# Kernel tuning notes

Hardware: AMD Instinct MI355X
Metric: run time of the kernel (lower is better)

Reference implementation:

```python
import jax, jax.numpy as jnp
import numpy as np

B, T, I, H = 1024, 2048, 12, 512


def setup_inputs() -> dict:
    key = jax.random.key(0)
    k1, k2, k3, k4 = jax.random.split(key, 4)
    s = 1.0 / np.sqrt(H)
    return {
        "history": jax.random.normal(k1, (B, T, I), dtype=jnp.float32),
        "w_ih": jax.random.normal(k2, (3 * H, I), dtype=jnp.float32) * s,
        "w_hh": jax.random.normal(k3, (3 * H, H), dtype=jnp.float32) * s,
        "w_out": jax.random.normal(k4, (2, H), dtype=jnp.float32) * s,
        "b_out": jnp.zeros((2,), dtype=jnp.float32),
    }


def reference(history, w_ih, w_hh, w_out, b_out):
    # GRUCell recurrence over T steps with per-step linear head (torch GRUCell math, bias=False)
    xs = jnp.transpose(history, (1, 0, 2))  # [T, B, I]
    h0 = jnp.zeros((history.shape[0], H), dtype=history.dtype)

    def step(h, x_t):
        gi = x_t @ w_ih.T            # [B, 3H]
        gh = h @ w_hh.T              # [B, 3H]
        i_r, i_z, i_n = jnp.split(gi, 3, axis=-1)
        h_r, h_z, h_n = jnp.split(gh, 3, axis=-1)
        r = jax.nn.sigmoid(i_r + h_r)
        z = jax.nn.sigmoid(i_z + h_z)
        n = jnp.tanh(i_n + r * h_n)
        h_new = (1.0 - z) * n + z * h
        logit = h_new @ w_out.T + b_out  # [B, 2]
        return h_new, logit

    h_final, logits = jax.lax.scan(step, h0, xs)
    return jnp.transpose(logits, (1, 0, 2)), h_final  # ([B, T, 2], [B, H])
```

## Files before the change

### kernel.cpp

```cpp
#include <hip/hip_runtime.h>
#include <stdint.h>


#define NB 256
#define NT 256
#define TB 1024
#define TT 2048
#define II 12
#define HH 512
#define NCL 32
#define GBLK 8
#define ROWS 32

#define HTILE_B (ROWS * HH * 2)
#define HBUF_B  ((size_t)NCL * HTILE_B)
#define BAR_OFF ((size_t)2 * HBUF_B)
#define WS_USED (BAR_OFF + (size_t)NCL * 256)

#define LDSB (ROWS * 1024)

#define GAS __attribute__((address_space(1)))
#define LAS __attribute__((address_space(3)))

typedef _Float16 half8 __attribute__((ext_vector_type(8)));
typedef float    f32x4 __attribute__((ext_vector_type(4)));

static __device__ __forceinline__ float fast_sigmoid(float x) {
  float e = exp2f(-1.44269504f * x);
  return __builtin_amdgcn_rcpf(1.0f + e);
}
static __device__ __forceinline__ float fast_tanh(float x) {
  float e = exp2f(2.88539008f * x);
  return 1.0f - 2.0f * __builtin_amdgcn_rcpf(1.0f + e);
}

static __device__ __forceinline__ void wait_flags32(unsigned* f, unsigned tgt,
                                                    int* dead) {
  const int l = threadIdx.x & 63;
  long spin = 0;
  for (;;) {
    unsigned v = __hip_atomic_load(f + (l & 31), __ATOMIC_RELAXED,
                                   __HIP_MEMORY_SCOPE_AGENT);
    if (__all(v >= tgt)) break;
    if (++spin > (1L << 24)) { *dead = 1; break; }
  }
}

__global__ void __launch_bounds__(NT, 1)
gru_persistent(const float* __restrict__ hist,
               const float* __restrict__ w_ih,
               const float* __restrict__ w_hh,
               const float* __restrict__ w_out,
               const float* __restrict__ b_out,
               float* __restrict__ out,
               uint8_t* __restrict__ ws)
{
  extern __shared__ char smem[];
  char* ldsA = smem;
  const int bid = blockIdx.x;
  const int c   = bid & 31;
  const int g   = bid >> 5;
  const int tid = threadIdx.x;
  const int w   = tid >> 6;
  const int l   = tid & 63;
  const int l15 = l & 15;
  const int l4  = l >> 4;
  const int crb = c * ROWS;
  unsigned* loF = (unsigned*)(ws + BAR_OFF) + (size_t)c * 64;
  unsigned* hiF = loF + 32;
  const int myflag = g * 4 + w;

  const int col0 = g * 64 + w * 16;

  half8 wr[16], wz[16], wn[16];
#pragma unroll
  for (int ks = 0; ks < 16; ++ks) {
    const size_t Rr = (size_t)(0 * HH + col0 + l15) * HH + ks * 32 + l4 * 8;
    const size_t Rz = (size_t)(1 * HH + col0 + l15) * HH + ks * 32 + l4 * 8;
    const size_t Rn = (size_t)(2 * HH + col0 + l15) * HH + ks * 32 + l4 * 8;
#pragma unroll
    for (int i = 0; i < 8; ++i) {
      wr[ks][i] = (_Float16)w_hh[Rr + i];
      wz[ks][i] = (_Float16)w_hh[Rz + i];
      wn[ks][i] = (_Float16)w_hh[Rn + i];
    }
  }

  half8 wih[3];
#pragma unroll
  for (int gt = 0; gt < 3; ++gt) {
    const int R = gt * HH + col0 + l15;
#pragma unroll
    for (int i = 0; i < 8; ++i) {
      const int k = l4 * 8 + i;
      wih[gt][i] = (_Float16)((k < II) ? w_ih[R * II + k] : 0.0f);
    }
  }

  const int jj = (l >> 4) & 1;
  float wor[32];
#pragma unroll
  for (int i = 0; i < 32; ++i) wor[i] = w_out[jj * HH + l15 * 32 + i];
  const float bo = b_out[jj];

  float hprev[2][4];
#pragma unroll
  for (int mt = 0; mt < 2; ++mt)
#pragma unroll
    for (int q = 0; q < 4; ++q) hprev[mt][q] = 0.0f;

  const int pcol = col0 + l15;
  int deadlock = 0;

  f32x4 xn0[2], xn1[2];
#pragma unroll
  for (int mt = 0; mt < 2; ++mt) {
    xn0[mt] = (f32x4){0.f, 0.f, 0.f, 0.f};
    xn1[mt] = (f32x4){0.f, 0.f, 0.f, 0.f};
    const float* xp = hist + (size_t)(crb + mt * 16 + l15) * (TT * II);
    if (l4 == 0)      { xn0[mt] = *(const f32x4*)xp; xn1[mt] = *(const f32x4*)(xp + 4); }
    else if (l4 == 1) { xn0[mt] = *(const f32x4*)(xp + 8); }
  }

  unsigned preLo = 0, preHi = 0;

  for (int t = 0; t < TT; ++t) {
    const uint8_t* hsrc = ws + ((t & 1) ? HBUF_B : 0) + (size_t)c * HTILE_B;
    uint8_t*       hdst = ws + ((t & 1) ? 0 : HBUF_B) + (size_t)c * HTILE_B;

    if (!__all(preLo >= (unsigned)t)) wait_flags32(loF, (unsigned)t, &deadlock);
    __builtin_amdgcn_sched_barrier(0);

#pragma unroll
    for (int it = 0; it < 4; ++it)
      __builtin_amdgcn_global_load_lds(
          (const GAS uint32_t*)(hsrc + it * 4096 + tid * 16),
          (LAS uint32_t*)(ldsA + it * 4096 + tid * 16), 16, 0, 17);
    __builtin_amdgcn_sched_barrier(0);

    half8 ax[2];
#pragma unroll
    for (int mt = 0; mt < 2; ++mt)
#pragma unroll
      for (int i = 0; i < 4; ++i) {
        ax[mt][i]     = (_Float16)xn0[mt][i];
        ax[mt][4 + i] = (_Float16)xn1[mt][i];
      }
    {
      const int tx = (t + 1 < TT) ? (t + 1) : 0;
#pragma unroll
      for (int mt = 0; mt < 2; ++mt) {
        const float* xp = hist + (size_t)(crb + mt * 16 + l15) * (TT * II) + (size_t)tx * II;
        if (l4 == 0)      { xn0[mt] = *(const f32x4*)xp; xn1[mt] = *(const f32x4*)(xp + 4); }
        else if (l4 == 1) { xn0[mt] = *(const f32x4*)(xp + 8); }
      }
    }
    preHi = __hip_atomic_load(hiF + (l & 31), __ATOMIC_RELAXED,
                              __HIP_MEMORY_SCOPE_AGENT);
    __builtin_amdgcn_sched_barrier(0);

    asm volatile("s_waitcnt vmcnt(7)" ::: "memory");
    __builtin_amdgcn_s_barrier();
    __builtin_amdgcn_sched_barrier(0);

    f32x4 acc0 = (f32x4){0.f, 0.f, 0.f, 0.f};
    f32x4 acc1 = acc0, acc2 = acc0;
    f32x4 accin = __builtin_amdgcn_mfma_f32_16x16x32_f16(ax[0], wih[2],
                    (f32x4){0.f, 0.f, 0.f, 0.f}, 0, 0, 0);
    acc0 = __builtin_amdgcn_mfma_f32_16x16x32_f16(ax[0], wih[0], acc0, 0, 0, 0);
    acc1 = __builtin_amdgcn_mfma_f32_16x16x32_f16(ax[0], wih[1], acc1, 0, 0, 0);
#pragma unroll
    for (int ks = 0; ks < 16; ++ks) {
      const int ko = (ks * 64 + l4 * 16) ^ ((l15 & 7) << 4);
      half8 a = *(const half8*)(ldsA + l15 * 1024 + ko);
      acc0 = __builtin_amdgcn_mfma_f32_16x16x32_f16(a, wr[ks], acc0, 0, 0, 0);
      acc1 = __builtin_amdgcn_mfma_f32_16x16x32_f16(a, wz[ks], acc1, 0, 0, 0);
      acc2 = __builtin_amdgcn_mfma_f32_16x16x32_f16(a, wn[ks], acc2, 0, 0, 0);
    }

    if (!__all(preHi >= (unsigned)t)) wait_flags32(hiF, (unsigned)t, &deadlock);
    __builtin_amdgcn_sched_barrier(0);
#pragma unroll
    for (int it = 0; it < 4; ++it)
      __builtin_amdgcn_global_load_lds(
          (const GAS uint32_t*)(hsrc + 16384 + it * 4096 + tid * 16),
          (LAS uint32_t*)(ldsA + 16384 + it * 4096 + tid * 16), 16, 0, 17);
    __builtin_amdgcn_sched_barrier(0);

#pragma unroll
    for (int q = 0; q < 4; ++q) {
      const int m = l4 * 4 + q;
      const float r  = fast_sigmoid(acc0[q]);
      const float z  = fast_sigmoid(acc1[q]);
      const float n  = fast_tanh(accin[q] + r * acc2[q]);
      const float hn = (1.0f - z) * n + z * hprev[0][q];
      hprev[0][q] = hn;
      const unsigned short hu = __builtin_bit_cast(unsigned short, (_Float16)hn);
      __hip_atomic_store(
          (unsigned short*)(hdst + m * 1024 + ((pcol * 2) ^ ((m & 7) << 4))),
          hu, __ATOMIC_RELAXED, __HIP_MEMORY_SCOPE_AGENT);
    }
    __builtin_amdgcn_sched_barrier(0);

    asm volatile("s_waitcnt vmcnt(0)" ::: "memory");
    if (l == 0)
      __hip_atomic_store(loF + myflag, (unsigned)(t + 1), __ATOMIC_RELAXED,
                         __HIP_MEMORY_SCOPE_AGENT);
    __builtin_amdgcn_s_barrier();
    __builtin_amdgcn_sched_barrier(0);

    acc0 = (f32x4){0.f, 0.f, 0.f, 0.f};
    acc1 = acc0; acc2 = acc0;
    accin = __builtin_amdgcn_mfma_f32_16x16x32_f16(ax[1], wih[2],
              (f32x4){0.f, 0.f, 0.f, 0.f}, 0, 0, 0);
    acc0 = __builtin_amdgcn_mfma_f32_16x16x32_f16(ax[1], wih[0], acc0, 0, 0, 0);
    acc1 = __builtin_amdgcn_mfma_f32_16x16x32_f16(ax[1], wih[1], acc1, 0, 0, 0);
#pragma unroll
    for (int ks = 0; ks < 16; ++ks) {
      const int ko = (ks * 64 + l4 * 16) ^ ((l15 & 7) << 4);
      half8 a = *(const half8*)(ldsA + (16 + l15) * 1024 + ko);
      acc0 = __builtin_amdgcn_mfma_f32_16x16x32_f16(a, wr[ks], acc0, 0, 0, 0);
      acc1 = __builtin_amdgcn_mfma_f32_16x16x32_f16(a, wz[ks], acc1, 0, 0, 0);
      acc2 = __builtin_amdgcn_mfma_f32_16x16x32_f16(a, wn[ks], acc2, 0, 0, 0);
    }
#pragma unroll
    for (int q = 0; q < 4; ++q) {
      const int m = 16 + l4 * 4 + q;
      const float r  = fast_sigmoid(acc0[q]);
      const float z  = fast_sigmoid(acc1[q]);
      const float n  = fast_tanh(accin[q] + r * acc2[q]);
      const float hn = (1.0f - z) * n + z * hprev[1][q];
      hprev[1][q] = hn;
      const unsigned short hu = __builtin_bit_cast(unsigned short, (_Float16)hn);
      __hip_atomic_store(
          (unsigned short*)(hdst + m * 1024 + ((pcol * 2) ^ ((m & 7) << 4))),
          hu, __ATOMIC_RELAXED, __HIP_MEMORY_SCOPE_AGENT);
    }

    if (t > 0) {
      const int lr  = g * 4 + w;
      const int row = crb + lr;
      float s = 0.0f;
#pragma unroll
      for (int c8 = 0; c8 < 4; ++c8) {
        half8 hv = *(const half8*)(ldsA + lr * 1024 +
                                   ((l15 * 64 + c8 * 16) ^ ((lr & 7) << 4)));
#pragma unroll
        for (int i = 0; i < 8; ++i) s += (float)hv[i] * wor[c8 * 8 + i];
      }
#pragma unroll
      for (int off = 1; off < 16; off <<= 1) s += __shfl_xor(s, off);
      if (l15 == 0 && l < 32) out[((size_t)row * TT + (t - 1)) * 2 + jj] = s + bo;
    }

    asm volatile("s_waitcnt vmcnt(0)" ::: "memory");
    if (l == 0)
      __hip_atomic_store(hiF + myflag, (unsigned)(t + 1), __ATOMIC_RELAXED,
                         __HIP_MEMORY_SCOPE_AGENT);
    preLo = __hip_atomic_load(loF + (l & 31), __ATOMIC_RELAXED,
                              __HIP_MEMORY_SCOPE_AGENT);
  }

  wait_flags32(loF, (unsigned)TT, &deadlock);
  wait_flags32(hiF, (unsigned)TT, &deadlock);
  {
    const uint8_t* hsrc = ws + ((TT & 1) ? HBUF_B : 0) + (size_t)c * HTILE_B;
#pragma unroll
    for (int it = 0; it < 8; ++it)
      __builtin_amdgcn_global_load_lds(
          (const GAS uint32_t*)(hsrc + it * 4096 + tid * 16),
          (LAS uint32_t*)(ldsA + it * 4096 + tid * 16), 16, 0, 17);
    asm volatile("s_waitcnt vmcnt(0)" ::: "memory");
    __builtin_amdgcn_s_barrier();

    const int lr  = g * 4 + w;
    const int row = crb + lr;
    float s = 0.0f;
#pragma unroll
    for (int c8 = 0; c8 < 4; ++c8) {
      half8 hv = *(const half8*)(ldsA + lr * 1024 +
                                 ((l15 * 64 + c8 * 16) ^ ((lr & 7) << 4)));
#pragma unroll
      for (int i = 0; i < 8; ++i) s += (float)hv[i] * wor[c8 * 8 + i];
    }
#pragma unroll
    for (int off = 1; off < 16; off <<= 1) s += __shfl_xor(s, off);
    if (l15 == 0 && l < 32) out[((size_t)row * TT + (TT - 1)) * 2 + jj] = s + bo;
  }

#pragma unroll
  for (int mt = 0; mt < 2; ++mt)
#pragma unroll
    for (int q = 0; q < 4; ++q) {
      const int m = mt * 16 + l4 * 4 + q;
      out[(size_t)TB * TT * 2 + (size_t)(crb + m) * HH + pcol] = hprev[mt][q];
    }
}

extern "C" void kernel_launch(void* const* d_in, const int* in_sizes, int n_in,
                              void* d_out, int out_size, void* d_ws, size_t ws_size,
                              hipStream_t stream) {
  (void)in_sizes; (void)n_in; (void)out_size;
  if (ws_size < WS_USED) return;

  const float* hist  = (const float*)d_in[0];
  const float* w_ih  = (const float*)d_in[1];
  const float* w_hh  = (const float*)d_in[2];
  const float* w_out = (const float*)d_in[3];
  const float* b_out = (const float*)d_in[4];
  float* out = (float*)d_out;
  uint8_t* ws = (uint8_t*)d_ws;

  hipMemsetAsync(d_ws, 0, WS_USED, stream);

  void* args[] = {(void*)&hist, (void*)&w_ih, (void*)&w_hh, (void*)&w_out,
                  (void*)&b_out, (void*)&out, (void*)&ws};
  hipError_t e = hipLaunchCooperativeKernel((const void*)gru_persistent,
                                            dim3(NB), dim3(NT), args,
                                            (unsigned)LDSB, stream);
  if (e != hipSuccess) {
    gru_persistent<<<dim3(NB), dim3(NT), LDSB, stream>>>(
        hist, w_ih, w_hh, w_out, b_out, out, ws);
  }
}
```

Measured before the change: 8.727 ms.

## Issue both h-tile halves before first MFMA phase and split output head per half

The wait on the high-half flags and the load of the second half of the hidden-state tile into LDS now happen before the first matmul phase instead of between the two phases. That takes the second-half load latency and flag wait off the critical path between phases. The output-head dot product is remapped so each wave handles one row and one output in each half, using 8 weights per lane and a full-wave reduction. This spreads the head work across both phases and shrinks register use. In exchange, the first phase now stalls until every producer has published the high half, which may serialize cross-block progress.

```diff
diff --git a/kernel.cpp b/kernel.cpp
--- a/kernel.cpp
+++ b/kernel.cpp
@@ -9,7 +9,6 @@
 #define II 12
 #define HH 512
 #define NCL 32
-#define GBLK 8
 #define ROWS 32
 
 #define HTILE_B (ROWS * HH * 2)
@@ -71,6 +70,7 @@
   const int myflag = g * 4 + w;
 
   const int col0 = g * 64 + w * 16;
+  const int pcol = col0 + l15;
 
   half8 wr[16], wz[16], wn[16];
 #pragma unroll
@@ -97,10 +97,11 @@
     }
   }
 
-  const int jj = (l >> 4) & 1;
-  float wor[32];
-#pragma unroll
-  for (int i = 0; i < 32; ++i) wor[i] = w_out[jj * HH + l15 * 32 + i];
+  const int jj   = myflag & 1;
+  const int erow = myflag >> 1;
+  float wor8[8];
+#pragma unroll
+  for (int i = 0; i < 8; ++i) wor8[i] = w_out[jj * HH + l * 8 + i];
   const float bo = b_out[jj];
 
   float hprev[2][4];
@@ -109,7 +110,6 @@
 #pragma unroll
     for (int q = 0; q < 4; ++q) hprev[mt][q] = 0.0f;
 
-  const int pcol = col0 + l15;
   int deadlock = 0;
 
   f32x4 xn0[2], xn1[2];
@@ -121,6 +121,7 @@
     if (l4 == 0)      { xn0[mt] = *(const f32x4*)xp; xn1[mt] = *(const f32x4*)(xp + 4); }
     else if (l4 == 1) { xn0[mt] = *(const f32x4*)(xp + 8); }
   }
+  asm volatile("s_waitcnt vmcnt(0)" ::: "memory");
 
   unsigned preLo = 0, preHi = 0;
 
@@ -128,7 +129,9 @@
     const uint8_t* hsrc = ws + ((t & 1) ? HBUF_B : 0) + (size_t)c * HTILE_B;
     uint8_t*       hdst = ws + ((t & 1) ? 0 : HBUF_B) + (size_t)c * HTILE_B;
 
-    if (!__all(preLo >= (unsigned)t)) wait_flags32(loF, (unsigned)t, &deadlock);
+    if (t > 0) {
+      if (!__all(preLo >= (unsigned)t)) wait_flags32(loF, (unsigned)t, &deadlock);
+    }
     __builtin_amdgcn_sched_barrier(0);
 
 #pragma unroll
@@ -138,6 +141,9 @@
           (LAS uint32_t*)(ldsA + it * 4096 + tid * 16), 16, 0, 17);
     __builtin_amdgcn_sched_barrier(0);
 
+    preHi = __hip_atomic_load(hiF + (l & 31), __ATOMIC_RELAXED,
+                              __HIP_MEMORY_SCOPE_AGENT);
+    __builtin_amdgcn_sched_barrier(0);
     half8 ax[2];
 #pragma unroll
     for (int mt = 0; mt < 2; ++mt)
@@ -155,11 +161,20 @@
         else if (l4 == 1) { xn0[mt] = *(const f32x4*)(xp + 8); }
       }
     }
-    preHi = __hip_atomic_load(hiF + (l & 31), __ATOMIC_RELAXED,
-                              __HIP_MEMORY_SCOPE_AGENT);
-    __builtin_amdgcn_sched_barrier(0);
-
-    asm volatile("s_waitcnt vmcnt(7)" ::: "memory");
+    __builtin_amdgcn_sched_barrier(0);
+
+    asm volatile("s_waitcnt vmcnt(6)" ::: "memory");
+    __builtin_amdgcn_sched_barrier(0);
+    if (t > 0 && !__all(preHi >= (unsigned)t)) wait_flags32(hiF, (unsigned)t, &deadlock);
+    __builtin_amdgcn_sched_barrier(0);
+
+#pragma unroll
+    for (int it = 0; it < 4; ++it)
+      __builtin_amdgcn_global_load_lds(
+          (const GAS uint32_t*)(hsrc + 16384 + it * 4096 + tid * 16),
+          (LAS uint32_t*)(ldsA + 16384 + it * 4096 + tid * 16), 16, 0, 17);
+    __builtin_amdgcn_sched_barrier(0);
+
     __builtin_amdgcn_s_barrier();
     __builtin_amdgcn_sched_barrier(0);
 
@@ -177,15 +192,6 @@
       acc1 = __builtin_amdgcn_mfma_f32_16x16x32_f16(a, wz[ks], acc1, 0, 0, 0);
       acc2 = __builtin_amdgcn_mfma_f32_16x16x32_f16(a, wn[ks], acc2, 0, 0, 0);
     }
-
-    if (!__all(preHi >= (unsigned)t)) wait_flags32(hiF, (unsigned)t, &deadlock);
-    __builtin_amdgcn_sched_barrier(0);
-#pragma unroll
-    for (int it = 0; it < 4; ++it)
-      __builtin_amdgcn_global_load_lds(
-          (const GAS uint32_t*)(hsrc + 16384 + it * 4096 + tid * 16),
-          (LAS uint32_t*)(ldsA + 16384 + it * 4096 + tid * 16), 16, 0, 17);
-    __builtin_amdgcn_sched_barrier(0);
 
 #pragma unroll
     for (int q = 0; q < 4; ++q) {
@@ -195,17 +201,29 @@
       const float n  = fast_tanh(accin[q] + r * acc2[q]);
       const float hn = (1.0f - z) * n + z * hprev[0][q];
       hprev[0][q] = hn;
-      const unsigned short hu = __builtin_bit_cast(unsigned short, (_Float16)hn);
       __hip_atomic_store(
           (unsigned short*)(hdst + m * 1024 + ((pcol * 2) ^ ((m & 7) << 4))),
-          hu, __ATOMIC_RELAXED, __HIP_MEMORY_SCOPE_AGENT);
+          __builtin_bit_cast(unsigned short, (_Float16)hn),
+          __ATOMIC_RELAXED, __HIP_MEMORY_SCOPE_AGENT);
+    }
+
+    if (t > 0) {
+      float s = 0.0f;
+      half8 hv = *(const half8*)(ldsA + erow * 1024 + ((l * 16) ^ ((erow & 7) << 4)));
+#pragma unroll
+      for (int i = 0; i < 8; ++i) s += (float)hv[i] * wor8[i];
+#pragma unroll
+      for (int off = 1; off < 64; off <<= 1) s += __shfl_xor(s, off);
+      if (l == 0) out[((size_t)(crb + erow) * TT + (t - 1)) * 2 + jj] = s + bo;
     }
     __builtin_amdgcn_sched_barrier(0);
 
     asm volatile("s_waitcnt vmcnt(0)" ::: "memory");
+    __builtin_amdgcn_sched_barrier(0);
     if (l == 0)
       __hip_atomic_store(loF + myflag, (unsigned)(t + 1), __ATOMIC_RELAXED,
                          __HIP_MEMORY_SCOPE_AGENT);
+
     __builtin_amdgcn_s_barrier();
     __builtin_amdgcn_sched_barrier(0);
 
@@ -231,29 +249,26 @@
       const float n  = fast_tanh(accin[q] + r * acc2[q]);
       const float hn = (1.0f - z) * n + z * hprev[1][q];
       hprev[1][q] = hn;
-      const unsigned short hu = __builtin_bit_cast(unsigned short, (_Float16)hn);
       __hip_atomic_store(
           (unsigned short*)(hdst + m * 1024 + ((pcol * 2) ^ ((m & 7) << 4))),
-          hu, __ATOMIC_RELAXED, __HIP_MEMORY_SCOPE_AGENT);
+          __builtin_bit_cast(unsigned short, (_Float16)hn),
+          __ATOMIC_RELAXED, __HIP_MEMORY_SCOPE_AGENT);
     }
 
     if (t > 0) {
-      const int lr  = g * 4 + w;
-      const int row = crb + lr;
+      const int lrw = 16 + erow;
       float s = 0.0f;
-#pragma unroll
-      for (int c8 = 0; c8 < 4; ++c8) {
-        half8 hv = *(const half8*)(ldsA + lr * 1024 +
-                                   ((l15 * 64 + c8 * 16) ^ ((lr & 7) << 4)));
-#pragma unroll
-        for (int i = 0; i < 8; ++i) s += (float)hv[i] * wor[c8 * 8 + i];
-      }
-#pragma unroll
-      for (int off = 1; off < 16; off <<= 1) s += __shfl_xor(s, off);
-      if (l15 == 0 && l < 32) out[((size_t)row * TT + (t - 1)) * 2 + jj] = s + bo;
-    }
+      half8 hv = *(const half8*)(ldsA + lrw * 1024 + ((l * 16) ^ ((lrw & 7) << 4)));
+#pragma unroll
+      for (int i = 0; i < 8; ++i) s += (float)hv[i] * wor8[i];
+#pragma unroll
+      for (int off = 1; off < 64; off <<= 1) s += __shfl_xor(s, off);
+      if (l == 0) out[((size_t)(crb + lrw) * TT + (t - 1)) * 2 + jj] = s + bo;
+    }
+    __builtin_amdgcn_sched_barrier(0);
 
     asm volatile("s_waitcnt vmcnt(0)" ::: "memory");
+    __builtin_amdgcn_sched_barrier(0);
     if (l == 0)
       __hip_atomic_store(hiF + myflag, (unsigned)(t + 1), __ATOMIC_RELAXED,
                          __HIP_MEMORY_SCOPE_AGENT);
@@ -261,6 +276,7 @@
                               __HIP_MEMORY_SCOPE_AGENT);
   }
 
+  asm volatile("s_waitcnt vmcnt(0)" ::: "memory");
   wait_flags32(loF, (unsigned)TT, &deadlock);
   wait_flags32(hiF, (unsigned)TT, &deadlock);
   {
@@ -273,19 +289,17 @@
     asm volatile("s_waitcnt vmcnt(0)" ::: "memory");
     __builtin_amdgcn_s_barrier();
 
-    const int lr  = g * 4 + w;
-    const int row = crb + lr;
-    float s = 0.0f;
-#pragma unroll
-    for (int c8 = 0; c8 < 4; ++c8) {
-      half8 hv = *(const half8*)(ldsA + lr * 1024 +
-                                 ((l15 * 64 + c8 * 16) ^ ((lr & 7) << 4)));
-#pragma unroll
-      for (int i = 0; i < 8; ++i) s += (float)hv[i] * wor[c8 * 8 + i];
-    }
-#pragma unroll
-    for (int off = 1; off < 16; off <<= 1) s += __shfl_xor(s, off);
-    if (l15 == 0 && l < 32) out[((size_t)row * TT + (TT - 1)) * 2 + jj] = s + bo;
+#pragma unroll
+    for (int half = 0; half < 2; ++half) {
+      const int lrw = half * 16 + erow;
+      float s = 0.0f;
+      half8 hv = *(const half8*)(ldsA + lrw * 1024 + ((l * 16) ^ ((lrw & 7) << 4)));
+#pragma unroll
+      for (int i = 0; i < 8; ++i) s += (float)hv[i] * wor8[i];
+#pragma unroll
+      for (int off = 1; off < 64; off <<= 1) s += __shfl_xor(s, off);
+      if (l == 0) out[((size_t)(crb + lrw) * TT + (TT - 1)) * 2 + jj] = s + bo;
+    }
   }
 
 #pragma unroll
```

Result: slower. 9.109 ms (+4.4%).
